# Performance work log

Measured on AMD Instinct MI355X. Metric: run time of the kernel, lower is better.

Reference implementation:

```python
import jax, jax.numpy as jnp
import numpy as np

NUM_HEADS = 8
HEAD_SIZE = 64
INPUT = 512
OUT = NUM_HEADS * HEAD_SIZE
B, S = 4, 2048


def setup_inputs() -> dict:
    key = jax.random.key(0)
    ks = jax.random.split(key, 6)
    return {
        "key": jax.random.normal(ks[0], (B, S, INPUT), dtype=jnp.float32),
        "key_mask": jnp.zeros((B, 1, 1, S), dtype=jnp.float32),
        "query": jax.random.normal(ks[1], (B, S, INPUT), dtype=jnp.float32),
        "value": jax.random.normal(ks[2], (B, S, INPUT), dtype=jnp.float32),
        "wq": jax.random.normal(ks[3], (INPUT, OUT), dtype=jnp.float32) * (INPUT ** -0.5),
        "wk": jax.random.normal(ks[4], (INPUT, OUT), dtype=jnp.float32) * (INPUT ** -0.5),
        "wv": jax.random.normal(ks[5], (INPUT, OUT), dtype=jnp.float32) * (INPUT ** -0.5),
    }


def _split_heads(x):
    # [B, S, H*hd] -> [B, H, S, hd]
    b, s, _ = x.shape
    return x.reshape(b, s, NUM_HEADS, HEAD_SIZE).transpose(0, 2, 1, 3)


def reference(key, key_mask, query, value, wq, wk, wv):
    q = _split_heads(query @ wq)   # [B,H,S,hd]
    k = _split_heads(key @ wk)
    v = _split_heads(value @ wv)
    scale = 1.0 / jnp.sqrt(jnp.asarray(HEAD_SIZE, q.dtype))
    logits = jnp.einsum('bhqd,bhkd->bhqk', q, k) * scale + key_mask
    attn = jax.nn.softmax(logits, axis=-1)
    out = jnp.einsum('bhqk,bhkd->bhqd', attn, v)  # [B,H,S,hd]
    out = out.transpose(0, 2, 1, 3).reshape(out.shape[0], out.shape[2], OUT)
    return out
```

## Files before the change

### kernel.cpp

```cpp
#include <hip/hip_runtime.h>

typedef _Float16 f16;
typedef f16 f16x8 __attribute__((ext_vector_type(8)));
typedef f16 f16x4 __attribute__((ext_vector_type(4)));
typedef f16 f16x2 __attribute__((ext_vector_type(2)));
typedef float f32x4 __attribute__((ext_vector_type(4)));
typedef unsigned int u32;

#define MFMA16(a, b, c) __builtin_amdgcn_mfma_f32_16x16x32_f16(a, b, c, 0, 0, 0)

#define BATCH 4
#define NHEADS 8
#define HDIM 64
#define SEQ 2048
#define DIN 512
#define DOUT 512
#define LOG2E 1.44269504f
#define C1 0.18033688f

__device__ __forceinline__ void gl_lds16(const void* g, const void* l) {
  __builtin_amdgcn_global_load_lds(
      (const __attribute__((address_space(1))) u32*)g,
      (__attribute__((address_space(3))) u32*)l, 16, 0, 0);
}

__device__ __forceinline__ float fexp2(float x) {
  float r;
  asm("v_exp_f32 %0, %1" : "=v"(r) : "v"(x));
  return r;
}

__device__ __forceinline__ f16x2 pk2(float a, float b) {
  return __builtin_bit_cast(f16x2, __builtin_amdgcn_cvt_pkrtz(a, b));
}

__device__ __forceinline__ f16x4 pk4(float a, float b, float c, float d) {
  f16x2 u0 = pk2(a, b), u1 = pk2(c, d);
  f16x4 r;
  r[0] = u0[0]; r[1] = u0[1]; r[2] = u1[0]; r[3] = u1[1];
  return r;
}

__global__ __launch_bounds__(256) void prep_w(
    const float* __restrict__ wq, const float* __restrict__ wk,
    const float* __restrict__ wv, f16* __restrict__ wT) {
  __shared__ float tile[64][65];
  const float* w = blockIdx.z == 0 ? wq : (blockIdx.z == 1 ? wk : wv);
  f16* out = wT + (size_t)blockIdx.z * DIN * DOUT;
  int k0 = blockIdx.x * 64, n0 = blockIdx.y * 64;
  int t = threadIdx.x;
  int c = t & 63, rb = t >> 6;
#pragma unroll
  for (int ph = 0; ph < 16; ++ph) {
    int r = ph * 4 + rb;
    tile[r][c] = w[(size_t)(k0 + r) * DOUT + n0 + c];
  }
  __syncthreads();
#pragma unroll
  for (int ph = 0; ph < 16; ++ph) {
    int n = ph * 4 + rb;
    out[(size_t)(n0 + n) * DIN + k0 + c] = (f16)tile[c][n];
  }
}

__global__ __launch_bounds__(256, 3) void qkv_gemm(
    const float* __restrict__ xq, const float* __restrict__ xk,
    const float* __restrict__ xv, const f16* __restrict__ wT,
    f16* __restrict__ Qo, f16* __restrict__ Ko, f16* __restrict__ Vt) {
  __shared__ __attribute__((aligned(16))) f16 As[128 * 64];
  __shared__ __attribute__((aligned(16))) f16 Bs[128 * 64];
  int gemm = blockIdx.z;
  const float* x = gemm == 0 ? xq : (gemm == 1 ? xk : xv);
  const f16* wt = wT + (size_t)gemm * DIN * DOUT;
  int bx = blockIdx.x;
  int m0 = (bx & 63) * 128, n0 = (bx >> 6) * 128;
  int t = threadIdx.x, w = t >> 6, lane = t & 63;
  int lr = lane & 15, lq = lane >> 4;
  int wm = (w >> 1) * 64, wn = (w & 1) * 64;

  int tr = t >> 4, tc = t & 15;
  const float* xg = x + (size_t)(m0 + tr) * DIN + tc * 4;
  int aw[8];
#pragma unroll
  for (int ph = 0; ph < 8; ++ph) {
    int r = tr + 16 * ph;
    int phys = (tc >> 1) ^ (r & 7);
    aw[ph] = r * 64 + phys * 8 + (tc & 1) * 4;
  }

  int srow = lane >> 3;
  int schunk = (lane & 7) ^ srow;
  const f16* gb[4];
  const f16* lbb[4];
#pragma unroll
  for (int j = 0; j < 4; ++j) {
    int br = w * 32 + j * 8;
    gb[j] = wt + (size_t)(n0 + br + srow) * DIN + schunk * 8;
    lbb[j] = &Bs[__builtin_amdgcn_readfirstlane(br * 64)];
  }
  int xo0 = ((0 * 4 + lq) ^ (lr & 7)) * 8;
  int xo1 = ((1 * 4 + lq) ^ (lr & 7)) * 8;

  f32x4 zero = {0.f, 0.f, 0.f, 0.f};
  f32x4 acc[4][4];
#pragma unroll
  for (int i = 0; i < 4; ++i)
#pragma unroll
    for (int j = 0; j < 4; ++j) acc[i][j] = zero;

  for (int k0 = 0; k0 < DIN; k0 += 64) {
    __syncthreads();
#pragma unroll
    for (int j = 0; j < 4; ++j) gl_lds16(gb[j] + k0, lbb[j]);
#pragma unroll
    for (int ph = 0; ph < 8; ++ph) {
      float4 a = *(const float4*)(xg + (size_t)ph * 16 * DIN + k0);
      *(f16x4*)&As[aw[ph]] = pk4(a.x, a.y, a.z, a.w);
    }
    __syncthreads();
#pragma unroll
    for (int c = 0; c < 2; ++c) {
      int xo = c ? xo1 : xo0;
      f16x8 xf[4], wf[4];
#pragma unroll
      for (int i = 0; i < 4; ++i)
        xf[i] = *(const f16x8*)&As[(wm + i * 16 + lr) * 64 + xo];
#pragma unroll
      for (int i = 0; i < 4; ++i)
        wf[i] = *(const f16x8*)&Bs[(wn + i * 16 + lr) * 64 + xo];
      if (gemm == 2) {
#pragma unroll
        for (int i = 0; i < 4; ++i)
#pragma unroll
          for (int j = 0; j < 4; ++j)
            acc[i][j] = MFMA16(xf[i], wf[j], acc[i][j]);
      } else {
#pragma unroll
        for (int i = 0; i < 4; ++i)
#pragma unroll
          for (int j = 0; j < 4; ++j)
            acc[i][j] = MFMA16(wf[i], xf[j], acc[i][j]);
      }
    }
  }

  if (gemm == 2) {
#pragma unroll
    for (int i = 0; i < 4; ++i) {
#pragma unroll
      for (int j = 0; j < 4; ++j) {
        int m = m0 + wm + i * 16 + lq * 4;
        int n = n0 + wn + j * 16 + lr;
        int b = m >> 11, s = m & 2047;
        int h = n >> 6, d = n & 63;
        *(f16x4*)&Vt[(((size_t)b * NHEADS + h) * HDIM + d) * SEQ + s] =
            pk4(acc[i][j][0], acc[i][j][1], acc[i][j][2], acc[i][j][3]);
      }
    }
  } else {
    f16* O = gemm == 0 ? Qo : Ko;
    float sc = gemm == 0 ? C1 : 1.0f;
#pragma unroll
    for (int i = 0; i < 4; ++i) {
#pragma unroll
      for (int j = 0; j < 4; ++j) {
        int sg = m0 + wm + j * 16 + lr;
        int nd = n0 + wn + i * 16 + lq * 4;
        int b = sg >> 11, s = sg & 2047;
        int h = nd >> 6, d = nd & 63;
        *(f16x4*)&O[(((size_t)b * NHEADS + h) * SEQ + s) * HDIM + d] =
            pk4(acc[i][j][0] * sc, acc[i][j][1] * sc, acc[i][j][2] * sc,
                acc[i][j][3] * sc);
      }
    }
  }
}

__global__ __launch_bounds__(256, 2) void flash_attn(
    const f16* __restrict__ Q, const f16* __restrict__ K,
    const f16* __restrict__ Vt, const float* __restrict__ mask,
    float* __restrict__ out) {
  __shared__ __attribute__((aligned(16))) f16 Ks[128 * 64];
  __shared__ __attribute__((aligned(16))) f16 Vs[64 * 128];
  __shared__ __attribute__((aligned(16))) f16 Ps[128 * 136];

  int bh = blockIdx.x, q0 = blockIdx.y * 128;
  int b = bh >> 3, h = bh & 7;
  int t = threadIdx.x, w = t >> 6, lane = t & 63;
  int lr = lane & 15, lq = lane >> 4;

  const f16* Qg = Q + (size_t)bh * SEQ * HDIM;
  const f16* Kg = K + (size_t)bh * SEQ * HDIM;
  const f16* Vg = Vt + (size_t)bh * HDIM * SEQ;
  const float* mg = mask + (size_t)b * SEQ;

  f16x8 qf[2][2];
#pragma unroll
  for (int u = 0; u < 2; ++u)
#pragma unroll
    for (int c = 0; c < 2; ++c)
      qf[u][c] = *(const f16x8*)(Qg +
                                 (size_t)(q0 + w * 32 + u * 16 + lr) * HDIM +
                                 c * 32 + lq * 8);

  int krow = lane >> 3;
  int kchunk = (lane & 7) ^ krow;
  const f16* gk[4];
  const f16* gv[4];
  const f16* lk[4];
  const f16* lv[4];
#pragma unroll
  for (int j = 0; j < 4; ++j) {
    int kbr = w * 32 + j * 8;
    gk[j] = Kg + (size_t)(kbr + krow) * HDIM + kchunk * 8;
    lk[j] = &Ks[__builtin_amdgcn_readfirstlane(kbr * 64)];
    int vbr = w * 16 + j * 4;
    int vchunk = (lane & 15) ^ (j * 4 + lq);
    gv[j] = Vg + (size_t)(vbr + lq) * SEQ + vchunk * 8;
    lv[j] = &Vs[__builtin_amdgcn_readfirstlane(vbr * 128)];
  }
  int xk0 = ((0 * 4 + lq) ^ (lr & 7)) * 8;
  int xk1 = ((1 * 4 + lq) ^ (lr & 7)) * 8;

  f32x4 zero = {0.f, 0.f, 0.f, 0.f};
  f32x4 acc[2][4];
#pragma unroll
  for (int u = 0; u < 2; ++u)
#pragma unroll
    for (int i = 0; i < 4; ++i) acc[u][i] = zero;
  float lsum[2] = {0.f, 0.f};

  for (int k0 = 0; k0 < SEQ; k0 += 128) {
    __syncthreads();
#pragma unroll
    for (int j = 0; j < 4; ++j) {
      gl_lds16(gk[j] + (size_t)k0 * HDIM, lk[j]);
      gl_lds16(gv[j] + k0, lv[j]);
    }
    __syncthreads();

    f32x4 s[2][8];
#pragma unroll
    for (int nt = 0; nt < 8; ++nt) {
      f16x8 kf0 = *(const f16x8*)&Ks[(nt * 16 + lr) * 64 + xk0];
      f16x8 kf1 = *(const f16x8*)&Ks[(nt * 16 + lr) * 64 + xk1];
      s[0][nt] = MFMA16(kf0, qf[0][0], zero);
      s[0][nt] = MFMA16(kf1, qf[0][1], s[0][nt]);
      s[1][nt] = MFMA16(kf0, qf[1][0], zero);
      s[1][nt] = MFMA16(kf1, qf[1][1], s[1][nt]);
    }

#pragma unroll
    for (int nt = 0; nt < 8; ++nt) {
      float4 mk = *(const float4*)(mg + k0 + nt * 16 + lq * 4);
#pragma unroll
      for (int u = 0; u < 2; ++u) {
        float p0 = fexp2(fmaf(mk.x, LOG2E, s[u][nt][0]));
        float p1 = fexp2(fmaf(mk.y, LOG2E, s[u][nt][1]));
        float p2 = fexp2(fmaf(mk.z, LOG2E, s[u][nt][2]));
        float p3 = fexp2(fmaf(mk.w, LOG2E, s[u][nt][3]));
        lsum[u] += (p0 + p1) + (p2 + p3);
        *(f16x4*)&Ps[(w * 32 + u * 16 + lr) * 136 + nt * 16 + lq * 4] =
            pk4(p0, p1, p2, p3);
      }
    }

#pragma unroll
    for (int ks = 0; ks < 4; ++ks) {
      f16x8 ap0 = *(const f16x8*)&Ps[(w * 32 + lr) * 136 + ks * 32 + lq * 8];
      f16x8 ap1 =
          *(const f16x8*)&Ps[(w * 32 + 16 + lr) * 136 + ks * 32 + lq * 8];
#pragma unroll
      for (int dt = 0; dt < 4; ++dt) {
        f16x8 bv = *(const f16x8*)&Vs[(dt * 16 + lr) * 128 +
                                      (((ks * 4 + lq) ^ lr) * 8)];
        acc[0][dt] = MFMA16(ap0, bv, acc[0][dt]);
        acc[1][dt] = MFMA16(ap1, bv, acc[1][dt]);
      }
    }
  }

#pragma unroll
  for (int u = 0; u < 2; ++u) {
    float l = lsum[u];
    l += __shfl_xor(l, 16);
    l += __shfl_xor(l, 32);
    float inv = 1.f / l;
    float iv[4];
#pragma unroll
    for (int r = 0; r < 4; ++r) iv[r] = __shfl(inv, lq * 4 + r);
#pragma unroll
    for (int dt = 0; dt < 4; ++dt) {
#pragma unroll
      for (int r = 0; r < 4; ++r) {
        int q = q0 + w * 32 + u * 16 + lq * 4 + r;
        int d = h * HDIM + dt * 16 + lr;
        out[((size_t)b * SEQ + q) * DOUT + d] = acc[u][dt][r] * iv[r];
      }
    }
  }
}

extern "C" void kernel_launch(void* const* d_in, const int* in_sizes, int n_in,
                              void* d_out, int out_size, void* d_ws,
                              size_t ws_size, hipStream_t stream) {
  const float* key = (const float*)d_in[0];
  const float* key_mask = (const float*)d_in[1];
  const float* query = (const float*)d_in[2];
  const float* value = (const float*)d_in[3];
  const float* wq = (const float*)d_in[4];
  const float* wk = (const float*)d_in[5];
  const float* wv = (const float*)d_in[6];
  float* out = (float*)d_out;

  char* ws = (char*)d_ws;
  f16* Qws = (f16*)(ws);
  f16* Kws = (f16*)(ws + 8388608);
  f16* Vtws = (f16*)(ws + 16777216);
  f16* wT = (f16*)(ws + 25165824);

  prep_w<<<dim3(8, 8, 3), 256, 0, stream>>>(wq, wk, wv, wT);
  qkv_gemm<<<dim3(256, 1, 3), 256, 0, stream>>>(query, key, value, wT, Qws,
                                                Kws, Vtws);
  flash_attn<<<dim3(32, 16), 256, 0, stream>>>(Qws, Kws, Vtws, key_mask, out);
}
```

Before: 188.2 us.

## Double-buffer weight tiles and prefetch activations in the QKV GEMM loop

The QKV projection GEMM now uses two LDS buffers for the weight tile. It also keeps the next step's fp32 activations in registers, so the global loads for step k+1 are issued before the MFMA work of step k. This is meant to hide global memory latency behind compute instead of stalling at each iteration's barrier. The cost is 16 KB more LDS per block and about 32 extra VGPRs per thread, which could lower occupancy under the 3-blocks launch bound.

```diff
diff --git a/kernel.cpp b/kernel.cpp
--- a/kernel.cpp
+++ b/kernel.cpp
@@ -67,8 +67,11 @@
     const float* __restrict__ xq, const float* __restrict__ xk,
     const float* __restrict__ xv, const f16* __restrict__ wT,
     f16* __restrict__ Qo, f16* __restrict__ Ko, f16* __restrict__ Vt) {
-  __shared__ __attribute__((aligned(16))) f16 As[128 * 64];
-  __shared__ __attribute__((aligned(16))) f16 Bs[128 * 64];
+  __shared__ __attribute__((aligned(16))) f16 smem[24576];
+  f16* As = smem;
+  f16* Bs0 = smem + 8192;
+  f16* Bs1 = smem + 16384;
+
   int gemm = blockIdx.z;
   const float* x = gemm == 0 ? xq : (gemm == 1 ? xk : xv);
   const f16* wt = wT + (size_t)gemm * DIN * DOUT;
@@ -91,12 +94,12 @@
   int srow = lane >> 3;
   int schunk = (lane & 7) ^ srow;
   const f16* gb[4];
-  const f16* lbb[4];
+  int lbo[4];
 #pragma unroll
   for (int j = 0; j < 4; ++j) {
     int br = w * 32 + j * 8;
     gb[j] = wt + (size_t)(n0 + br + srow) * DIN + schunk * 8;
-    lbb[j] = &Bs[__builtin_amdgcn_readfirstlane(br * 64)];
+    lbo[j] = __builtin_amdgcn_readfirstlane(br * 64);
   }
   int xo0 = ((0 * 4 + lq) ^ (lr & 7)) * 8;
   int xo1 = ((1 * 4 + lq) ^ (lr & 7)) * 8;
@@ -108,16 +111,29 @@
 #pragma unroll
     for (int j = 0; j < 4; ++j) acc[i][j] = zero;
 
-  for (int k0 = 0; k0 < DIN; k0 += 64) {
+  float4 ar[8];
+#pragma unroll
+  for (int j = 0; j < 4; ++j) gl_lds16(gb[j], Bs0 + lbo[j]);
+#pragma unroll
+  for (int ph = 0; ph < 8; ++ph)
+    ar[ph] = *(const float4*)(xg + (size_t)ph * 16 * DIN);
+
+  for (int it = 0; it < 8; ++it) {
+    f16* Bc = (it & 1) ? Bs1 : Bs0;
+    f16* Bn = (it & 1) ? Bs0 : Bs1;
     __syncthreads();
 #pragma unroll
-    for (int j = 0; j < 4; ++j) gl_lds16(gb[j] + k0, lbb[j]);
-#pragma unroll
-    for (int ph = 0; ph < 8; ++ph) {
-      float4 a = *(const float4*)(xg + (size_t)ph * 16 * DIN + k0);
-      *(f16x4*)&As[aw[ph]] = pk4(a.x, a.y, a.z, a.w);
-    }
+    for (int ph = 0; ph < 8; ++ph)
+      *(f16x4*)&As[aw[ph]] = pk4(ar[ph].x, ar[ph].y, ar[ph].z, ar[ph].w);
     __syncthreads();
+    if (it < 7) {
+      int k1 = (it + 1) * 64;
+#pragma unroll
+      for (int j = 0; j < 4; ++j) gl_lds16(gb[j] + k1, Bn + lbo[j]);
+#pragma unroll
+      for (int ph = 0; ph < 8; ++ph)
+        ar[ph] = *(const float4*)(xg + (size_t)ph * 16 * DIN + k1);
+    }
 #pragma unroll
     for (int c = 0; c < 2; ++c) {
       int xo = c ? xo1 : xo0;
@@ -127,7 +143,7 @@
         xf[i] = *(const f16x8*)&As[(wm + i * 16 + lr) * 64 + xo];
 #pragma unroll
       for (int i = 0; i < 4; ++i)
-        wf[i] = *(const f16x8*)&Bs[(wn + i * 16 + lr) * 64 + xo];
+        wf[i] = *(const f16x8*)&Bc[(wn + i * 16 + lr) * 64 + xo];
       if (gemm == 2) {
 #pragma unroll
         for (int i = 0; i < 4; ++i)
```

Result: slower. 269.7 us (+43.3%).
